# Kernel optimization log

Hardware: AMD Instinct MI355X
Metric: run time of the kernel (lower is better)

## Reference

```python
import jax, jax.numpy as jnp
import numpy as np

LAYERS = [2048, 2048, 2048, 512]
THRESHOLD = 1.0
TAU_MEM = 20.0
TAU_SYN = 5.0
DT = 1.0
BATCH = 32
T = 100


def setup_inputs() -> dict:
    key = jax.random.key(0)
    ks = jax.random.split(key, 2 + 2 * (len(LAYERS) - 1))
    inp = {
        "x": jax.random.uniform(ks[0], (BATCH, LAYERS[0]), dtype=jnp.float32),
        "noise": jax.random.uniform(ks[1], (T, BATCH, LAYERS[0]), dtype=jnp.float32),
        "time_steps": T,
    }
    # nn.Linear-style init: U(-1/sqrt(fan_in), 1/sqrt(fan_in))
    for i in range(len(LAYERS) - 1):
        fan_in, fan_out = LAYERS[i], LAYERS[i + 1]
        bound = 1.0 / np.sqrt(fan_in)
        inp[f"W{i}"] = jax.random.uniform(ks[2 + 2 * i], (fan_out, fan_in), minval=-bound, maxval=bound, dtype=jnp.float32)
        inp[f"b{i}"] = jax.random.uniform(ks[3 + 2 * i], (fan_out,), minval=-bound, maxval=bound, dtype=jnp.float32)
    return inp


def _lif_step(I, mem, syn):
    # dI_syn/dt = -I_syn/tau_syn + I ; dV/dt = -V/tau_mem + I_syn  (explicit Euler, dt=1)
    syn = syn + (-syn / TAU_SYN + I) * DT
    mem = mem + (-mem / TAU_MEM + syn) * DT
    spikes = (mem >= THRESHOLD).astype(mem.dtype)
    mem = mem * (1.0 - spikes)          # reset fired neurons
    mem = mem * (mem > 0).astype(mem.dtype)  # clamp negative potentials to 0
    return spikes, mem, syn


def reference(x, noise, W0, b0, W1, b1, W2, b2, time_steps):
    params = [(W0, b0), (W1, b1), (W2, b2)]
    batch = x.shape[0]
    dtype = x.dtype
    rate = jnp.clip(x, 0.0, 1.0)                       # [B, in]
    in_spikes = (noise < rate[None]).astype(dtype)     # [T, B, in] Poisson encoding

    mems = tuple(jnp.zeros((batch, W.shape[0]), dtype) for W, _ in params)
    syns = tuple(jnp.zeros((batch, W.shape[0]), dtype) for W, _ in params)

    def step(carry, sp_in):
        mems, syns = carry
        layer_in = sp_in
        new_mems, new_syns = [], []
        count = jnp.zeros((), dtype)
        for (W, b), m, s in zip(params, mems, syns):
            I = layer_in @ W.T + b
            spk, m, s = _lif_step(I, m, s)
            new_mems.append(m)
            new_syns.append(s)
            count = count + spk.sum()
            layer_in = spk
        return (tuple(new_mems), tuple(new_syns)), (layer_in, count)

    (_, _), (out_spikes, counts) = jax.lax.scan(step, (mems, syns), in_spikes)
    output = out_spikes.mean(axis=0)   # [B, out]: time-averaged output spike train
    total_spikes = counts.sum()
    return output, total_spikes
```

## Files before the change

kernel.cpp:

```cpp
#include <hip/hip_runtime.h>

#define T_STEPS 100
#define MTOT    3200
#define R0_OFF  0
#define R1_OFF  13107200
#define I_OFF   26214400

typedef _Float16 half8_t __attribute__((ext_vector_type(8)));
typedef _Float16 half4_t __attribute__((ext_vector_type(4)));
typedef float    f32x4   __attribute__((ext_vector_type(4)));

__device__ __forceinline__ void encode_body(
    int blk, const float* __restrict__ x, const float* __restrict__ noise,
    _Float16* __restrict__ spk0, float* __restrict__ out)
{
    if (blk == 0 && threadIdx.x == 0) out[16384] = 0.0f;
    const int tid = threadIdx.x;
    const int m0  = blk * 16;
    __shared__ half8_t lds[16 * 257];
    #pragma unroll
    for (int ml = 0; ml < 16; ++ml) {
        const int m = m0 + ml;
        const int t = m >> 5, b = m & 31;
        const float4 x1 = *(const float4*)(x + b * 2048 + tid * 8);
        const float4 x2 = *(const float4*)(x + b * 2048 + tid * 8 + 4);
        const float4 n1 = *(const float4*)(noise + (size_t)t * 65536 + b * 2048 + tid * 8);
        const float4 n2 = *(const float4*)(noise + (size_t)t * 65536 + b * 2048 + tid * 8 + 4);
        const float xr[8] = {x1.x,x1.y,x1.z,x1.w,x2.x,x2.y,x2.z,x2.w};
        const float nz[8] = {n1.x,n1.y,n1.z,n1.w,n2.x,n2.y,n2.z,n2.w};
        half8_t sp;
        #pragma unroll
        for (int j = 0; j < 8; ++j) {
            const float r = fminf(fmaxf(xr[j], 0.0f), 1.0f);
            sp[j] = (nz[j] < r) ? (_Float16)1.0f : (_Float16)0.0f;
        }
        lds[ml * 257 + tid] = sp;
    }
    __syncthreads();
    #pragma unroll
    for (int r = 0; r < 16; ++r) {
        const int ml  = tid & 15;
        const int oct = r * 16 + (tid >> 4);
        *(half8_t*)(spk0 + ((size_t)oct * MTOT + m0 + ml) * 8) = lds[ml * 257 + oct];
    }
}

__device__ __forceinline__ void convw_body(
    int blk, const float* __restrict__ W, _Float16* __restrict__ Wf)
{
    const int koct = threadIdx.x;
    #pragma unroll
    for (int r = 0; r < 8; ++r) {
        const int row = blk * 8 + r;
        const float* wp = W + (size_t)row * 2048 + koct * 8;
        const float4 f1 = *(const float4*)(wp);
        const float4 f2 = *(const float4*)(wp + 4);
        half8_t h = {(_Float16)f1.x,(_Float16)f1.y,(_Float16)f1.z,(_Float16)f1.w,
                     (_Float16)f2.x,(_Float16)f2.y,(_Float16)f2.z,(_Float16)f2.w};
        const size_t idx = (size_t)(row >> 4) * 32768
                         + ((size_t)((koct >> 2) * 64 + (koct & 3) * 16 + (row & 15))) * 8;
        *(half8_t*)(Wf + idx) = h;
    }
}

__device__ __forceinline__ void scan_body(
    int blk, const _Float16* __restrict__ I, const float* __restrict__ bias,
    _Float16* __restrict__ spk_out, float* __restrict__ out,
    const int nshift, const int is_last)
{
    const int gid = blk * 256 + threadIdx.x;
    const int N = 1 << nshift;
    const int n = gid & (N - 1);
    const int b = gid >> nshift;
    const float bi = bias[n];
    const size_t nbase = (size_t)(n >> 3) * (MTOT * 8) + (n & 7);
    float mem = 0.f, syn = 0.f, osum = 0.f, cnt = 0.f;
    #pragma unroll 4
    for (int t = 0; t < T_STEPS; ++t) {
        const int m = t * 32 + b;
        const float Iv = (float)I[nbase + (size_t)m * 8] + bi;
        syn = syn + (-syn / 5.0f + Iv);
        mem = mem + (-mem / 20.0f + syn);
        const float sv = (mem >= 1.0f) ? 1.0f : 0.0f;
        mem = (sv != 0.0f) ? 0.0f : mem;
        mem = (mem > 0.0f) ? mem : 0.0f;
        cnt += sv; osum += sv;
        if (!is_last) spk_out[nbase + (size_t)m * 8] = (_Float16)sv;
    }
    if (is_last) out[b * 512 + n] = osum * 0.01f;
    float c = cnt;
    #pragma unroll
    for (int s2 = 1; s2 < 64; s2 <<= 1) c += __shfl_xor(c, s2);
    if ((threadIdx.x & 63) == 0) atomicAdd(&out[16384], c);
}

__global__ __launch_bounds__(256, 2) void snn_enc_convw_kernel(
    const float* __restrict__ x, const float* __restrict__ noise,
    _Float16* __restrict__ spk0, float* __restrict__ out,
    const float* __restrict__ W, _Float16* __restrict__ Wf)
{
    if (blockIdx.x < 200) encode_body(blockIdx.x, x, noise, spk0, out);
    else                  convw_body(blockIdx.x - 200, W, Wf);
}

__global__ __launch_bounds__(256, 4) void snn_scan_convw_kernel(
    const _Float16* __restrict__ I, const float* __restrict__ bias,
    _Float16* __restrict__ spk_out, float* __restrict__ out,
    const int scan_blocks, const int nshift,
    const float* __restrict__ W, _Float16* __restrict__ Wf)
{
    if ((int)blockIdx.x < scan_blocks)
        scan_body(blockIdx.x, I, bias, spk_out, out, nshift, 0);
    else
        convw_body(blockIdx.x - scan_blocks, W, Wf);
}

__global__ __launch_bounds__(256, 4) void snn_scan_kernel(
    const _Float16* __restrict__ I, const float* __restrict__ bias,
    float* __restrict__ out, const int nshift)
{
    scan_body(blockIdx.x, I, bias, nullptr, out, nshift, 1);
}

template<int NC, int TPW>
__global__ __launch_bounds__(1024, 4) void snn_gemm_kernel(
    const _Float16* __restrict__ Wf, const _Float16* __restrict__ spk,
    _Float16* __restrict__ I)
{
    const int tid  = threadIdx.x;
    const int lane = tid & 63;
    const int w    = tid >> 6;
    const int quad = lane >> 4, mi = lane & 15;
    const int chunk = blockIdx.x % NC;
    const int nbb   = blockIdx.x / NC;
    const int row_base = nbb * 32;
    const int jcount = (200 - chunk + NC - 1) / NC;

    __shared__ _Float16 wlds[32 * 2048];
    {
        const half8_t* __restrict__ src = (const half8_t*)(Wf + (size_t)nbb * 65536);
        half8_t* __restrict__ dst = (half8_t*)wlds;
        #pragma unroll
        for (int r = 0; r < 8; ++r) dst[tid + r * 1024] = src[tid + r * 1024];
    }
    __syncthreads();

    for (int jl0 = TPW * w; jl0 < jcount; jl0 += 16 * TPW) {
        int mt[TPW]; bool val[TPW];
        const _Float16* bp[TPW];
        #pragma unroll
        for (int u = 0; u < TPW; ++u) {
            const int jl = jl0 + u;
            val[u] = jl < jcount;
            mt[u]  = chunk + NC * (val[u] ? jl : jl0);
            bp[u]  = spk + ((size_t)mt[u] * 16 + mi) * 8;
        }
        f32x4 acc[TPW][2];
        #pragma unroll
        for (int u = 0; u < TPW; ++u) { acc[u][0] = (f32x4){0,0,0,0}; acc[u][1] = (f32x4){0,0,0,0}; }

        half8_t bc[TPW];
        const size_t k0 = (size_t)quad * (MTOT * 8);
        #pragma unroll
        for (int u = 0; u < TPW; ++u) bc[u] = *(const half8_t*)(bp[u] + k0);

        #pragma unroll 4
        for (int kb = 0; kb < 64; ++kb) {
            half8_t bn[TPW];
            if (kb < 63) {
                const size_t kn = (size_t)((kb + 1) * 4 + quad) * (MTOT * 8);
                #pragma unroll
                for (int u = 0; u < TPW; ++u) bn[u] = *(const half8_t*)(bp[u] + kn);
            }
            const half8_t a0 = *(const half8_t*)(wlds + ((size_t)(kb * 64 + lane)) * 8);
            const half8_t a1 = *(const half8_t*)(wlds + 32768 + ((size_t)(kb * 64 + lane)) * 8);
            #pragma unroll
            for (int u = 0; u < TPW; ++u) {
                acc[u][0] = __builtin_amdgcn_mfma_f32_16x16x32_f16(a0, bc[u], acc[u][0], 0, 0, 0);
                acc[u][1] = __builtin_amdgcn_mfma_f32_16x16x32_f16(a1, bc[u], acc[u][1], 0, 0, 0);
            }
            #pragma unroll
            for (int u = 0; u < TPW; ++u) bc[u] = bn[u];
        }
        #pragma unroll
        for (int s = 0; s < 2; ++s) {
            const int n0 = row_base + s * 16 + quad * 4;
            const size_t obase = (size_t)(n0 >> 3) * (MTOT * 8) + (n0 & 7);
            #pragma unroll
            for (int u = 0; u < TPW; ++u) {
                if (!val[u]) continue;
                half4_t h;
                #pragma unroll
                for (int r = 0; r < 4; ++r) h[r] = (_Float16)acc[u][s][r];
                *(half4_t*)(I + obase + (size_t)(mt[u] * 16 + mi) * 8) = h;
            }
        }
    }
}

extern "C" void kernel_launch(void* const* d_in, const int* in_sizes, int n_in,
                              void* d_out, int out_size, void* d_ws, size_t ws_size,
                              hipStream_t stream) {
    const float* x     = (const float*)d_in[0];
    const float* noise = (const float*)d_in[1];
    const float* W0 = (const float*)d_in[3];
    const float* b0 = (const float*)d_in[4];
    const float* W1 = (const float*)d_in[5];
    const float* b1 = (const float*)d_in[6];
    const float* W2 = (const float*)d_in[7];
    const float* b2 = (const float*)d_in[8];
    float* out = (float*)d_out;

    _Float16* R0 = (_Float16*)((char*)d_ws + R0_OFF);
    _Float16* R1 = (_Float16*)((char*)d_ws + R1_OFF);
    _Float16* Ib = (_Float16*)((char*)d_ws + I_OFF);

    snn_enc_convw_kernel<<<dim3(456), dim3(256), 0, stream>>>(x, noise, R0, out, W0, R1);
    snn_gemm_kernel<4, 4><<<dim3(256), dim3(1024), 0, stream>>>(R1, R0, Ib);
    snn_scan_convw_kernel<<<dim3(512), dim3(256), 0, stream>>>(Ib, b0, R1, out, 256, 11, W1, R0);
    snn_gemm_kernel<4, 4><<<dim3(256), dim3(1024), 0, stream>>>(R0, R1, Ib);
    snn_scan_convw_kernel<<<dim3(320), dim3(256), 0, stream>>>(Ib, b1, R0, out, 256, 11, W2, R1);
    snn_gemm_kernel<16, 1><<<dim3(256), dim3(1024), 0, stream>>>(R1, R0, Ib);
    snn_scan_kernel<<<dim3(64), dim3(256), 0, stream>>>(Ib, b2, out, 9);

    (void)in_sizes; (void)n_in; (void)out_size; (void)ws_size;
}
```

Measured before the change: 290.4 us.

## Balance GEMM tiles across waves and prefetch spike operands before weight staging

New measurement: 296.3 us. 1.02x slower.

```diff
diff --git a/kernel.cpp b/kernel.cpp
--- a/kernel.cpp
+++ b/kernel.cpp
@@ -122,6 +122,69 @@
     scan_body(blockIdx.x, I, bias, nullptr, out, nshift, 1);
 }
 
+
+template<int NT, int TPW>
+__device__ __forceinline__ void gemm_tiles(
+    const _Float16* __restrict__ wlds, _Float16* __restrict__ I,
+    const _Float16* const (&bp)[TPW], const int (&mt)[TPW],
+    half8_t (&pre0)[TPW], half8_t (&pre1)[TPW],
+    const int row_base, const int lane)
+{
+    const int quad = lane >> 4, mi = lane & 15;
+    f32x4 acc[NT][2];
+    #pragma unroll
+    for (int u = 0; u < NT; ++u) { acc[u][0] = (f32x4){0,0,0,0}; acc[u][1] = (f32x4){0,0,0,0}; }
+
+    half8_t bc0[NT], bc1[NT];
+    #pragma unroll
+    for (int u = 0; u < NT; ++u) { bc0[u] = pre0[u]; bc1[u] = pre1[u]; }
+
+    #pragma unroll 2
+    for (int kb = 0; kb < 64; kb += 2) {
+        half8_t bn0[NT], bn1[NT];
+        if (kb < 62) {
+            const size_t kn0 = (size_t)((kb + 2) * 4 + quad) * (MTOT * 8);
+            #pragma unroll
+            for (int u = 0; u < NT; ++u) bn0[u] = *(const half8_t*)(bp[u] + kn0);
+        }
+        const half8_t a00 = *(const half8_t*)(wlds + ((size_t)(kb * 64 + lane)) * 8);
+        const half8_t a01 = *(const half8_t*)(wlds + 32768 + ((size_t)(kb * 64 + lane)) * 8);
+        #pragma unroll
+        for (int u = 0; u < NT; ++u) {
+            acc[u][0] = __builtin_amdgcn_mfma_f32_16x16x32_f16(a00, bc0[u], acc[u][0], 0, 0, 0);
+            acc[u][1] = __builtin_amdgcn_mfma_f32_16x16x32_f16(a01, bc0[u], acc[u][1], 0, 0, 0);
+        }
+        if (kb < 62) {
+            const size_t kn1 = (size_t)((kb + 3) * 4 + quad) * (MTOT * 8);
+            #pragma unroll
+            for (int u = 0; u < NT; ++u) bn1[u] = *(const half8_t*)(bp[u] + kn1);
+        }
+        const half8_t a10 = *(const half8_t*)(wlds + ((size_t)((kb + 1) * 64 + lane)) * 8);
+        const half8_t a11 = *(const half8_t*)(wlds + 32768 + ((size_t)((kb + 1) * 64 + lane)) * 8);
+        #pragma unroll
+        for (int u = 0; u < NT; ++u) {
+            acc[u][0] = __builtin_amdgcn_mfma_f32_16x16x32_f16(a10, bc1[u], acc[u][0], 0, 0, 0);
+            acc[u][1] = __builtin_amdgcn_mfma_f32_16x16x32_f16(a11, bc1[u], acc[u][1], 0, 0, 0);
+        }
+        if (kb < 62) {
+            #pragma unroll
+            for (int u = 0; u < NT; ++u) { bc0[u] = bn0[u]; bc1[u] = bn1[u]; }
+        }
+    }
+    #pragma unroll
+    for (int s = 0; s < 2; ++s) {
+        const int n0 = row_base + s * 16 + quad * 4;
+        const size_t obase = (size_t)(n0 >> 3) * (MTOT * 8) + (n0 & 7);
+        #pragma unroll
+        for (int u = 0; u < NT; ++u) {
+            half4_t h;
+            #pragma unroll
+            for (int r = 0; r < 4; ++r) h[r] = (_Float16)acc[u][s][r];
+            *(half4_t*)(I + obase + (size_t)(mt[u] * 16 + mi) * 8) = h;
+        }
+    }
+}
+
 template<int NC, int TPW>
 __global__ __launch_bounds__(1024, 4) void snn_gemm_kernel(
     const _Float16* __restrict__ Wf, const _Float16* __restrict__ spk,
@@ -130,11 +193,28 @@
     const int tid  = threadIdx.x;
     const int lane = tid & 63;
     const int w    = tid >> 6;
-    const int quad = lane >> 4, mi = lane & 15;
+    const int mi   = lane & 15;
+    const int quad = lane >> 4;
     const int chunk = blockIdx.x % NC;
     const int nbb   = blockIdx.x / NC;
     const int row_base = nbb * 32;
     const int jcount = (200 - chunk + NC - 1) / NC;
+    const int rem    = jcount - 16 * (TPW - 1);
+    const int cnt      = (w < rem) ? TPW : (TPW - 1);
+    const int jl_start = w * (TPW - 1) + ((w < rem) ? w : rem);
+
+    int mt[TPW]; const _Float16* bp[TPW];
+    #pragma unroll
+    for (int u = 0; u < TPW; ++u) {
+        int jl = jl_start + u; if (jl > jcount - 1) jl = jcount - 1;
+        mt[u] = chunk + NC * jl;
+        bp[u] = spk + ((size_t)mt[u] * 16 + mi) * 8;
+    }
+    half8_t pre0[TPW], pre1[TPW];
+    #pragma unroll
+    for (int u = 0; u < TPW; ++u) pre0[u] = *(const half8_t*)(bp[u] + (size_t)quad * (MTOT * 8));
+    #pragma unroll
+    for (int u = 0; u < TPW; ++u) pre1[u] = *(const half8_t*)(bp[u] + (size_t)(4 + quad) * (MTOT * 8));
 
     __shared__ _Float16 wlds[32 * 2048];
     {
@@ -145,56 +225,10 @@
     }
     __syncthreads();
 
-    for (int jl0 = TPW * w; jl0 < jcount; jl0 += 16 * TPW) {
-        int mt[TPW]; bool val[TPW];
-        const _Float16* bp[TPW];
-        #pragma unroll
-        for (int u = 0; u < TPW; ++u) {
-            const int jl = jl0 + u;
-            val[u] = jl < jcount;
-            mt[u]  = chunk + NC * (val[u] ? jl : jl0);
-            bp[u]  = spk + ((size_t)mt[u] * 16 + mi) * 8;
-        }
-        f32x4 acc[TPW][2];
-        #pragma unroll
-        for (int u = 0; u < TPW; ++u) { acc[u][0] = (f32x4){0,0,0,0}; acc[u][1] = (f32x4){0,0,0,0}; }
-
-        half8_t bc[TPW];
-        const size_t k0 = (size_t)quad * (MTOT * 8);
-        #pragma unroll
-        for (int u = 0; u < TPW; ++u) bc[u] = *(const half8_t*)(bp[u] + k0);
-
-        #pragma unroll 4
-        for (int kb = 0; kb < 64; ++kb) {
-            half8_t bn[TPW];
-            if (kb < 63) {
-                const size_t kn = (size_t)((kb + 1) * 4 + quad) * (MTOT * 8);
-                #pragma unroll
-                for (int u = 0; u < TPW; ++u) bn[u] = *(const half8_t*)(bp[u] + kn);
-            }
-            const half8_t a0 = *(const half8_t*)(wlds + ((size_t)(kb * 64 + lane)) * 8);
-            const half8_t a1 = *(const half8_t*)(wlds + 32768 + ((size_t)(kb * 64 + lane)) * 8);
-            #pragma unroll
-            for (int u = 0; u < TPW; ++u) {
-                acc[u][0] = __builtin_amdgcn_mfma_f32_16x16x32_f16(a0, bc[u], acc[u][0], 0, 0, 0);
-                acc[u][1] = __builtin_amdgcn_mfma_f32_16x16x32_f16(a1, bc[u], acc[u][1], 0, 0, 0);
-            }
-            #pragma unroll
-            for (int u = 0; u < TPW; ++u) bc[u] = bn[u];
-        }
-        #pragma unroll
-        for (int s = 0; s < 2; ++s) {
-            const int n0 = row_base + s * 16 + quad * 4;
-            const size_t obase = (size_t)(n0 >> 3) * (MTOT * 8) + (n0 & 7);
-            #pragma unroll
-            for (int u = 0; u < TPW; ++u) {
-                if (!val[u]) continue;
-                half4_t h;
-                #pragma unroll
-                for (int r = 0; r < 4; ++r) h[r] = (_Float16)acc[u][s][r];
-                *(half4_t*)(I + obase + (size_t)(mt[u] * 16 + mi) * 8) = h;
-            }
-        }
+    if (cnt == TPW) {
+        gemm_tiles<TPW, TPW>(wlds, I, bp, mt, pre0, pre1, row_base, lane);
+    } else if constexpr (TPW >= 2) {
+        gemm_tiles<TPW - 1, TPW>(wlds, I, bp, mt, pre0, pre1, row_base, lane);
     }
 }
 
```

## Use 64-row weight tiles in two K-halves for the 2048-wide layer GEMMs

Applied to the files above, without the earlier changes.

Result: faster. 275.5 us (-5.1%).

```diff
diff --git a/kernel.cpp b/kernel.cpp
--- a/kernel.cpp
+++ b/kernel.cpp
@@ -122,6 +122,147 @@
     scan_body(blockIdx.x, I, bias, nullptr, out, nshift, 1);
 }
 
+
+__device__ __forceinline__ half8_t ldB(const _Float16* __restrict__ p, int kq) {
+    return *(const half8_t*)(p + (size_t)kq * (MTOT * 8));
+}
+
+template<bool HAS2, int KB>
+__device__ __forceinline__ void gemm64_half(
+    const _Float16* __restrict__ wlds,
+    const _Float16* const (&bp)[2],
+    half8_t (&bE)[2], half8_t (&bO)[2],
+    f32x4 (&acc)[2][4],
+    const int lane, const int quad)
+{
+    #pragma unroll 2
+    for (int kbl = 0; kbl < 32; kbl += 2) {
+        half8_t a[4];
+        #pragma unroll
+        for (int s = 0; s < 4; ++s)
+            a[s] = *(const half8_t*)(wlds + (size_t)s * 16384 + (size_t)(kbl * 64 + lane) * 8);
+        #pragma unroll
+        for (int s = 0; s < 4; ++s) {
+            acc[0][s] = __builtin_amdgcn_mfma_f32_16x16x32_f16(a[s], bE[0], acc[0][s], 0, 0, 0);
+            if (HAS2)
+                acc[1][s] = __builtin_amdgcn_mfma_f32_16x16x32_f16(a[s], bE[1], acc[1][s], 0, 0, 0);
+        }
+        if (KB + kbl + 2 < 64) {
+            const int kq = (KB + kbl + 2) * 4 + quad;
+            bE[0] = ldB(bp[0], kq);
+            if (HAS2) bE[1] = ldB(bp[1], kq);
+        }
+        half8_t c[4];
+        #pragma unroll
+        for (int s = 0; s < 4; ++s)
+            c[s] = *(const half8_t*)(wlds + (size_t)s * 16384 + (size_t)((kbl + 1) * 64 + lane) * 8);
+        #pragma unroll
+        for (int s = 0; s < 4; ++s) {
+            acc[0][s] = __builtin_amdgcn_mfma_f32_16x16x32_f16(c[s], bO[0], acc[0][s], 0, 0, 0);
+            if (HAS2)
+                acc[1][s] = __builtin_amdgcn_mfma_f32_16x16x32_f16(c[s], bO[1], acc[1][s], 0, 0, 0);
+        }
+        if (KB + kbl + 3 < 64) {
+            const int kq = (KB + kbl + 3) * 4 + quad;
+            bO[0] = ldB(bp[0], kq);
+            if (HAS2) bO[1] = ldB(bp[1], kq);
+        }
+    }
+}
+
+template<int NC>
+__global__ __launch_bounds__(1024, 4) void snn_gemm64_kernel(
+    const _Float16* __restrict__ Wf, const _Float16* __restrict__ spk,
+    _Float16* __restrict__ I)
+{
+    const int tid  = threadIdx.x;
+    const int lane = tid & 63;
+    const int w    = tid >> 6;
+    const int mi   = lane & 15;
+    const int quad = lane >> 4;
+    const int chunk = blockIdx.x % NC;
+    const int nbb   = blockIdx.x / NC;
+    const int row_base = nbb * 64;
+    const int jcount = (200 - chunk + NC - 1) / NC;
+    const int rem    = jcount - 16;
+    const bool has2  = (w < rem);
+    int jl_start = has2 ? (2 * w) : (w + (rem > 0 ? rem : 0));
+    if (jl_start < 0) jl_start = 0;
+    const bool active = jl_start < jcount;
+
+    int mt[2]; const _Float16* bp[2];
+    #pragma unroll
+    for (int u = 0; u < 2; ++u) {
+        int jl = jl_start + u;
+        if (jl >= jcount) jl = jcount - 1;
+        mt[u] = chunk + NC * jl;
+        bp[u] = spk + ((size_t)mt[u] * 16 + mi) * 8;
+    }
+
+    half8_t bE[2], bO[2];
+    if (active) {
+        bE[0] = ldB(bp[0], quad);
+        bO[0] = ldB(bp[0], 4 + quad);
+        if (has2) { bE[1] = ldB(bp[1], quad); bO[1] = ldB(bp[1], 4 + quad); }
+    }
+
+    __shared__ _Float16 wlds[65536];
+    const half8_t* __restrict__ wsrc = (const half8_t*)Wf;
+    {
+        half8_t* dst = (half8_t*)wlds;
+        #pragma unroll
+        for (int r = 0; r < 8; ++r) {
+            const int flat = r * 1024 + tid;
+            const int s = flat >> 11, off = flat & 2047;
+            dst[flat] = wsrc[(size_t)(4 * nbb + s) * 4096 + off];
+        }
+    }
+    __syncthreads();
+
+    f32x4 acc[2][4];
+    #pragma unroll
+    for (int u = 0; u < 2; ++u) {
+        #pragma unroll
+        for (int s = 0; s < 4; ++s) acc[u][s] = (f32x4){0,0,0,0};
+    }
+
+    if (active) {
+        if (has2) gemm64_half<true , 0>(wlds, bp, bE, bO, acc, lane, quad);
+        else      gemm64_half<false, 0>(wlds, bp, bE, bO, acc, lane, quad);
+    }
+    __syncthreads();
+    {
+        half8_t* dst = (half8_t*)wlds;
+        #pragma unroll
+        for (int r = 0; r < 8; ++r) {
+            const int flat = r * 1024 + tid;
+            const int s = flat >> 11, off = flat & 2047;
+            dst[flat] = wsrc[(size_t)(4 * nbb + s) * 4096 + 2048 + off];
+        }
+    }
+    __syncthreads();
+    if (active) {
+        if (has2) gemm64_half<true , 32>(wlds, bp, bE, bO, acc, lane, quad);
+        else      gemm64_half<false, 32>(wlds, bp, bE, bO, acc, lane, quad);
+    }
+
+    if (active) {
+        #pragma unroll
+        for (int s = 0; s < 4; ++s) {
+            const int n0 = row_base + s * 16 + quad * 4;
+            const size_t obase = (size_t)(n0 >> 3) * (MTOT * 8) + (n0 & 7);
+            #pragma unroll
+            for (int u = 0; u < 2; ++u) {
+                if (u == 1 && !has2) continue;
+                half4_t h;
+                #pragma unroll
+                for (int r = 0; r < 4; ++r) h[r] = (_Float16)acc[u][s][r];
+                *(half4_t*)(I + obase + (size_t)(mt[u] * 16 + mi) * 8) = h;
+            }
+        }
+    }
+}
+
 template<int NC, int TPW>
 __global__ __launch_bounds__(1024, 4) void snn_gemm_kernel(
     const _Float16* __restrict__ Wf, const _Float16* __restrict__ spk,
@@ -216,9 +357,9 @@
     _Float16* Ib = (_Float16*)((char*)d_ws + I_OFF);
 
     snn_enc_convw_kernel<<<dim3(456), dim3(256), 0, stream>>>(x, noise, R0, out, W0, R1);
-    snn_gemm_kernel<4, 4><<<dim3(256), dim3(1024), 0, stream>>>(R1, R0, Ib);
+    snn_gemm64_kernel<8><<<dim3(256), dim3(1024), 0, stream>>>(R1, R0, Ib);
     snn_scan_convw_kernel<<<dim3(512), dim3(256), 0, stream>>>(Ib, b0, R1, out, 256, 11, W1, R0);
-    snn_gemm_kernel<4, 4><<<dim3(256), dim3(1024), 0, stream>>>(R0, R1, Ib);
+    snn_gemm64_kernel<8><<<dim3(256), dim3(1024), 0, stream>>>(R0, R1, Ib);
     snn_scan_convw_kernel<<<dim3(320), dim3(256), 0, stream>>>(Ib, b1, R0, out, 256, 11, W2, R1);
     snn_gemm_kernel<16, 1><<<dim3(256), dim3(1024), 0, stream>>>(R1, R0, Ib);
     snn_scan_kernel<<<dim3(64), dim3(256), 0, stream>>>(Ib, b2, out, 9);
```

## Add 64-row GEMM kernel with split-K warps and async LDS weight staging

Applied to the files above, without the earlier changes.

After: 311.0 us. 1.07x slower.

```diff
diff --git a/kernel.cpp b/kernel.cpp
--- a/kernel.cpp
+++ b/kernel.cpp
@@ -2,6 +2,7 @@
 
 #define T_STEPS 100
 #define MTOT    3200
+#define MTOT8   25600
 #define R0_OFF  0
 #define R1_OFF  13107200
 #define I_OFF   26214400
@@ -122,6 +123,170 @@
     scan_body(blockIdx.x, I, bias, nullptr, out, nshift, 1);
 }
 
+
+__device__ __forceinline__ half8_t ldBo(
+    const _Float16* __restrict__ spk, const int voff, const int kq)
+{
+    return *(const half8_t*)(spk + (size_t)voff + (size_t)kq * MTOT8);
+}
+
+__device__ __forceinline__ void stage_half(
+    const _Float16* __restrict__ Wf, _Float16* __restrict__ wlds,
+    const int nbb, const int h, const int w, const int lane)
+{
+    #pragma unroll
+    for (int r = 0; r < 8; ++r) {
+        const int unit = r * 1024 + w * 64 + lane;
+        const int s = unit >> 11, off = unit & 2047;
+        const _Float16* src = Wf + (size_t)(4 * nbb + s) * 32768
+                            + (size_t)h * 16384 + (size_t)off * 8;
+        _Float16* dst = wlds + (size_t)unit * 8;
+        __builtin_amdgcn_global_load_lds(
+            (const __attribute__((address_space(1))) void*)src,
+            (__attribute__((address_space(3))) void*)dst, 16, 0, 0);
+    }
+}
+
+template<int NT, int H>
+__device__ __forceinline__ void compute_half(
+    const _Float16* __restrict__ wlds, const _Float16* __restrict__ spk,
+    const int (&voff)[NT], half8_t (&bE)[NT], half8_t (&bO)[NT],
+    f32x4 (&acc)[NT][4], const int lane, const int quad, const int kg)
+{
+    #pragma unroll
+    for (int j = 0; j < 16; ++j) {
+        half8_t a[4];
+        #pragma unroll
+        for (int s = 0; s < 4; ++s)
+            a[s] = *(const half8_t*)(wlds + (size_t)s * 16384
+                                    + (size_t)((kg * 16 + j) * 64 + lane) * 8);
+        if ((j & 1) == 0) {
+            #pragma unroll
+            for (int t = 0; t < NT; ++t) {
+                #pragma unroll
+                for (int s = 0; s < 4; ++s)
+                    acc[t][s] = __builtin_amdgcn_mfma_f32_16x16x32_f16(a[s], bE[t], acc[t][s], 0, 0, 0);
+            }
+            if (H == 0 || j + 2 < 16) {
+                const int kb = kg * 16 + ((j + 2 < 16) ? (H * 32 + j + 2) : (j + 18));
+                const int kq = kb * 4 + quad;
+                #pragma unroll
+                for (int t = 0; t < NT; ++t) bE[t] = ldBo(spk, voff[t], kq);
+            }
+        } else {
+            #pragma unroll
+            for (int t = 0; t < NT; ++t) {
+                #pragma unroll
+                for (int s = 0; s < 4; ++s)
+                    acc[t][s] = __builtin_amdgcn_mfma_f32_16x16x32_f16(a[s], bO[t], acc[t][s], 0, 0, 0);
+            }
+            if (H == 0 || j + 2 < 16) {
+                const int kb = kg * 16 + ((j + 2 < 16) ? (H * 32 + j + 2) : (j + 18));
+                const int kq = kb * 4 + quad;
+                #pragma unroll
+                for (int t = 0; t < NT; ++t) bO[t] = ldBo(spk, voff[t], kq);
+            }
+        }
+    }
+}
+
+template<int NT>
+__device__ __forceinline__ void gemm64k_run(
+    const _Float16* __restrict__ Wf, const _Float16* __restrict__ spk,
+    _Float16* __restrict__ I, _Float16* __restrict__ wlds,
+    const int chunk, const int nbb, const int jl_start,
+    const int w, const int lane, const int quad, const int mi,
+    const int kg, const int mg)
+{
+    const int row_base = nbb * 64;
+
+    int voff[NT];
+    #pragma unroll
+    for (int t = 0; t < NT; ++t)
+        voff[t] = ((chunk + 8 * (jl_start + t)) * 16 + mi) * 8;
+
+    half8_t bE[NT], bO[NT];
+    {
+        const int kq0 = (kg * 16) * 4 + quad;
+        #pragma unroll
+        for (int t = 0; t < NT; ++t) bE[t] = ldBo(spk, voff[t], kq0);
+        const int kq1 = kq0 + 4;
+        #pragma unroll
+        for (int t = 0; t < NT; ++t) bO[t] = ldBo(spk, voff[t], kq1);
+    }
+
+    f32x4 acc[NT][4];
+    #pragma unroll
+    for (int t = 0; t < NT; ++t) {
+        #pragma unroll
+        for (int s = 0; s < 4; ++s) acc[t][s] = (f32x4){0, 0, 0, 0};
+    }
+
+    stage_half(Wf, wlds, nbb, 0, w, lane);
+    __syncthreads();
+    compute_half<NT, 0>(wlds, spk, voff, bE, bO, acc, lane, quad, kg);
+    __syncthreads();
+    stage_half(Wf, wlds, nbb, 1, w, lane);
+    __syncthreads();
+    compute_half<NT, 1>(wlds, spk, voff, bE, bO, acc, lane, quad, kg);
+    __syncthreads();
+
+    f32x4* red = (f32x4*)wlds;
+    if (kg == 1) {
+        #pragma unroll
+        for (int t = 0; t < NT; ++t) {
+            #pragma unroll
+            for (int s = 0; s < 4; ++s)
+                red[(mg * 16 + t * 4 + s) * 64 + lane] = acc[t][s];
+        }
+    }
+    __syncthreads();
+    if (kg == 0) {
+        #pragma unroll
+        for (int t = 0; t < NT; ++t) {
+            #pragma unroll
+            for (int s = 0; s < 4; ++s)
+                acc[t][s] += red[(mg * 16 + t * 4 + s) * 64 + lane];
+        }
+        #pragma unroll
+        for (int s = 0; s < 4; ++s) {
+            const int n0 = row_base + s * 16 + quad * 4;
+            const size_t obase = (size_t)(n0 >> 3) * (MTOT * 8) + (n0 & 7);
+            #pragma unroll
+            for (int t = 0; t < NT; ++t) {
+                const int mt = chunk + 8 * (jl_start + t);
+                half4_t h;
+                #pragma unroll
+                for (int r = 0; r < 4; ++r) h[r] = (_Float16)acc[t][s][r];
+                *(half4_t*)(I + obase + (size_t)(mt * 16 + mi) * 8) = h;
+            }
+        }
+    }
+}
+
+__global__ __launch_bounds__(1024, 1) void snn_gemm64k_kernel(
+    const _Float16* __restrict__ Wf, const _Float16* __restrict__ spk,
+    _Float16* __restrict__ I)
+{
+    const int tid  = threadIdx.x;
+    const int lane = tid & 63;
+    const int w    = tid >> 6;
+    const int mi   = lane & 15;
+    const int quad = lane >> 4;
+    const int chunk = blockIdx.x & 7;
+    const int nbb   = blockIdx.x >> 3;
+    const int mg = w & 7;
+    const int kg = w >> 3;
+    const int jl_start = (mg == 0) ? 0 : (3 * mg + 1);
+
+    __shared__ _Float16 wlds[65536];
+
+    if (mg == 0)
+        gemm64k_run<4>(Wf, spk, I, wlds, chunk, nbb, jl_start, w, lane, quad, mi, kg, mg);
+    else
+        gemm64k_run<3>(Wf, spk, I, wlds, chunk, nbb, jl_start, w, lane, quad, mi, kg, mg);
+}
+
 template<int NC, int TPW>
 __global__ __launch_bounds__(1024, 4) void snn_gemm_kernel(
     const _Float16* __restrict__ Wf, const _Float16* __restrict__ spk,
@@ -216,9 +381,9 @@
     _Float16* Ib = (_Float16*)((char*)d_ws + I_OFF);
 
     snn_enc_convw_kernel<<<dim3(456), dim3(256), 0, stream>>>(x, noise, R0, out, W0, R1);
-    snn_gemm_kernel<4, 4><<<dim3(256), dim3(1024), 0, stream>>>(R1, R0, Ib);
+    snn_gemm64k_kernel<<<dim3(256), dim3(1024), 0, stream>>>(R1, R0, Ib);
     snn_scan_convw_kernel<<<dim3(512), dim3(256), 0, stream>>>(Ib, b0, R1, out, 256, 11, W1, R0);
-    snn_gemm_kernel<4, 4><<<dim3(256), dim3(1024), 0, stream>>>(R0, R1, Ib);
+    snn_gemm64k_kernel<<<dim3(256), dim3(1024), 0, stream>>>(R0, R1, Ib);
     snn_scan_convw_kernel<<<dim3(320), dim3(256), 0, stream>>>(Ib, b1, R0, out, 256, 11, W2, R1);
     snn_gemm_kernel<16, 1><<<dim3(256), dim3(1024), 0, stream>>>(R1, R0, Ib);
     snn_scan_kernel<<<dim3(64), dim3(256), 0, stream>>>(Ib, b2, out, 9);
```
